# Optimization experiments

Measured on AMD Instinct MI355X. Metric: run time of the kernel, lower is better.

Reference implementation:

```python
import jax, jax.numpy as jnp
import numpy as np

DT_RANK = 64
N_STATES = 16


def selective_scan(u, delta, A, B, C, D):
    # u,delta: [b,l,d]; A: [d,n]; B,C: [b,l,n]; D: [d]
    dA = jnp.einsum('bld,dn->bldn', delta, A)
    dB_u = jnp.einsum('bld,bld,bln->bldn', delta, u, B)
    # shifted exclusive suffix-sum: cum[t] = sum_{s=t+1}^{L-1} dA[s]
    dA_shift = jnp.concatenate([dA[:, 1:], jnp.zeros_like(dA[:, :1])], axis=1)
    dA_cumsum = jnp.exp(jnp.flip(jnp.cumsum(jnp.flip(dA_shift, axis=1), axis=1), axis=1))
    xs = jnp.cumsum(dB_u * dA_cumsum, axis=1) / (dA_cumsum + 1e-12)
    y = jnp.einsum('bldn,bln->bld', xs, C)
    return y + u * D


def setup_inputs() -> dict:
    key = jax.random.key(0)
    ks = jax.random.split(key, 6)
    b, l, d = 2, 1024, 1024
    dt_rank, n = DT_RANK, N_STATES
    x = jax.random.normal(ks[0], (b, l, d), dtype=jnp.float32)
    # Dense kernels with glorot-ish scale
    W_x = jax.random.normal(ks[1], (d, dt_rank + 2 * n), dtype=jnp.float32) * (1.0 / np.sqrt(d))
    W_dt = jax.random.normal(ks[2], (dt_rank, d), dtype=jnp.float32) * (1.0 / np.sqrt(dt_rank))
    b_dt = jnp.zeros((d,), dtype=jnp.float32)
    # A_log = log(repeat(1..n, d)) as in S6.__init__
    A_log = jnp.log(jnp.tile(jnp.arange(1, n + 1, dtype=jnp.float32)[None, :], (d, 1)))
    D = jnp.ones((d,), dtype=jnp.float32)
    W_out = jax.random.normal(ks[3], (d, d), dtype=jnp.float32) * (1.0 / np.sqrt(d))
    b_out = jnp.zeros((d,), dtype=jnp.float32)
    return {"x": x, "W_x": W_x, "W_dt": W_dt, "b_dt": b_dt,
            "A_log": A_log, "D": D, "W_out": W_out, "b_out": b_out}


def reference(x, W_x, W_dt, b_dt, A_log, D, W_out, b_out):
    n = A_log.shape[1]
    A = -jnp.exp(A_log)                     # [d,n]
    x_dbl = jnp.einsum('bld,de->ble', x, W_x)  # [b,l,dt_rank+2n]
    delta = x_dbl[..., :DT_RANK]
    B = x_dbl[..., DT_RANK:DT_RANK + n]
    C = x_dbl[..., DT_RANK + n:]
    delta = jax.nn.softplus(jnp.einsum('blr,rd->bld', delta, W_dt) + b_dt)
    y = selective_scan(x, delta, A, B, C, D)
    return jnp.einsum('bld,de->ble', y, W_out) + b_out
```

## Files before the change

kernel.cpp:

```cpp
#include <hip/hip_runtime.h>
#include <hip/hip_bf16.h>

#define LSEQ 1024
#define DMODEL 1024
#define NSTATE 16
#define DTRANK 64
#define ECOL 96
#define MTOT 2048

typedef short s16x8 __attribute__((ext_vector_type(8)));
typedef float f32x4 __attribute__((ext_vector_type(4)));

#if __has_builtin(__builtin_amdgcn_exp2f)
#define EXP2F(x) __builtin_amdgcn_exp2f(x)
#else
#define EXP2F(x) exp2f(x)
#endif
#define LOG2E 1.4426950408889634

__device__ inline unsigned short f2bf(float f) {
    unsigned int u = __builtin_bit_cast(unsigned int, f);
    u += 0x7FFFu + ((u >> 16) & 1u);
    return (unsigned short)(u >> 16);
}
__device__ inline float bf2f(unsigned short h) {
    unsigned int u = ((unsigned int)h) << 16;
    return __builtin_bit_cast(float, u);
}

__device__ inline f32x4 shflup4(f32x4 v, int off) {
    f32x4 r;
    r[0] = __shfl_up(v[0], off, 64);
    r[1] = __shfl_up(v[1], off, 64);
    r[2] = __shfl_up(v[2], off, 64);
    r[3] = __shfl_up(v[3], off, 64);
    return r;
}

__global__ __launch_bounds__(256) void k_prep(const float* __restrict__ x,
                                              const float* __restrict__ Wx,
                                              const float* __restrict__ Wdt,
                                              const float* __restrict__ Wout,
                                              unsigned short* __restrict__ xTbf,
                                              unsigned short* __restrict__ WxTh,
                                              unsigned short* __restrict__ WxTl,
                                              unsigned short* __restrict__ WdtTh,
                                              unsigned short* __restrict__ WdtTl,
                                              unsigned short* __restrict__ WbfT) {
    __shared__ float t[64][65];
    int id = blockIdx.x;
    int tid = threadIdx.x;
    if (id < 512) {
        int d0 = (id & 15) * 64, m0 = (id >> 4) * 64;
        int tx = tid & 63, ty = tid >> 6;
#pragma unroll
        for (int j = 0; j < 64; j += 4)
            t[ty + j][tx] = x[(size_t)(m0 + ty + j) * 1024 + d0 + tx];
        __syncthreads();
#pragma unroll
        for (int j = 0; j < 64; j += 4)
            xTbf[(size_t)(d0 + ty + j) * 2048 + m0 + tx] = f2bf(t[tx][ty + j]);
    } else if (id < 512 + 96) {
        int id2 = id - 512;
        int e0 = (id2 % 3) * 32, k0 = (id2 / 3) * 32;
        int tx = tid & 31, ty = tid >> 5;
#pragma unroll
        for (int j = 0; j < 32; j += 8)
            t[ty + j][tx] = Wx[(size_t)(k0 + ty + j) * 96 + e0 + tx];
        __syncthreads();
#pragma unroll
        for (int j = 0; j < 32; j += 8) {
            float v = t[tx][ty + j];
            unsigned short h = f2bf(v);
            WxTh[(size_t)(e0 + ty + j) * 1024 + k0 + tx] = h;
            WxTl[(size_t)(e0 + ty + j) * 1024 + k0 + tx] = f2bf(v - bf2f(h));
        }
    } else if (id < 512 + 96 + 64) {
        int id3 = id - (512 + 96);
        int d0 = (id3 & 31) * 32, r0 = (id3 >> 5) * 32;
        int tx = tid & 31, ty = tid >> 5;
#pragma unroll
        for (int j = 0; j < 32; j += 8)
            t[ty + j][tx] = Wdt[(size_t)(r0 + ty + j) * 1024 + d0 + tx];
        __syncthreads();
#pragma unroll
        for (int j = 0; j < 32; j += 8) {
            float v = t[tx][ty + j];
            unsigned short h = f2bf(v);
            WdtTh[(size_t)(d0 + ty + j) * 64 + r0 + tx] = h;
            WdtTl[(size_t)(d0 + ty + j) * 64 + r0 + tx] = f2bf(v - bf2f(h));
        }
    } else {
        int id4 = id - (512 + 96 + 64);
        int e0 = (id4 & 15) * 64, k0 = (id4 >> 4) * 64;
        int tx = tid & 63, ty = tid >> 6;
#pragma unroll
        for (int j = 0; j < 64; j += 4)
            t[ty + j][tx] = Wout[(size_t)(k0 + ty + j) * 1024 + e0 + tx];
        __syncthreads();
#pragma unroll
        for (int j = 0; j < 64; j += 4)
            WbfT[(size_t)(e0 + ty + j) * 1024 + k0 + tx] = f2bf(t[tx][ty + j]);
    }
}

__global__ __launch_bounds__(256) void k_xdbl3(const float* __restrict__ x,
                                               const unsigned short* __restrict__ WxTh,
                                               const unsigned short* __restrict__ WxTl,
                                               float* __restrict__ part) {
    __shared__ unsigned short Ah[32 * 64], Al[32 * 64];
    __shared__ unsigned short Bh[96 * 64], Bl[96 * 64];
    int bm = (blockIdx.x >> 2) * 32;
    int slice = blockIdx.x & 3;
    int tid = threadIdx.x, lane = tid & 63, w = tid >> 6;
    int wm = w >> 1, wn = w & 1;
    int r = lane & 15, kb = lane >> 4;

    f32x4 acc[3];
#pragma unroll
    for (int nf = 0; nf < 3; ++nf) acc[nf] = (f32x4){0.f, 0.f, 0.f, 0.f};

#pragma unroll 1
    for (int kc = 0; kc < 4; ++kc) {
        int kbase = slice * 256 + kc * 64;
        __syncthreads();
        {
            int row = tid >> 3, cc = tid & 7;
            size_t src = (size_t)(bm + row) * 1024 + kbase + cc * 8;
            float4 v0 = *(const float4*)&x[src];
            float4 v1 = *(const float4*)&x[src + 4];
            float vv[8] = {v0.x, v0.y, v0.z, v0.w, v1.x, v1.y, v1.z, v1.w};
            s16x8 h, lo;
#pragma unroll
            for (int j = 0; j < 8; ++j) {
                unsigned short hb = f2bf(vv[j]);
                h[j] = (short)hb;
                lo[j] = (short)f2bf(vv[j] - bf2f(hb));
            }
            int dstB = row * 128 + ((cc * 16) ^ ((row & 7) << 4));
            *(s16x8*)((char*)Ah + dstB) = h;
            *(s16x8*)((char*)Al + dstB) = lo;
        }
#pragma unroll
        for (int j = 0; j < 3; ++j) {
            int c = tid + j * 256;
            int row = c >> 3, cc = c & 7;
            size_t src = (size_t)row * 1024 + kbase + cc * 8;
            int dstB = row * 128 + ((cc * 16) ^ ((row & 7) << 4));
            *(s16x8*)((char*)Bh + dstB) = *(const s16x8*)&WxTh[src];
            *(s16x8*)((char*)Bl + dstB) = *(const s16x8*)&WxTl[src];
        }
        __syncthreads();
#pragma unroll
        for (int ks = 0; ks < 2; ++ks) {
            int sw = (ks * 64 + kb * 16) ^ ((r & 7) << 4);
            s16x8 a_h = *(const s16x8*)((char*)Ah + (wm * 16 + r) * 128 + sw);
            s16x8 a_l = *(const s16x8*)((char*)Al + (wm * 16 + r) * 128 + sw);
#pragma unroll
            for (int nf = 0; nf < 3; ++nf) {
                int brow = wn * 48 + nf * 16 + r;
                s16x8 b_h = *(const s16x8*)((char*)Bh + brow * 128 + sw);
                s16x8 b_l = *(const s16x8*)((char*)Bl + brow * 128 + sw);
                acc[nf] = __builtin_amdgcn_mfma_f32_16x16x32_bf16(a_h, b_h, acc[nf], 0, 0, 0);
                acc[nf] = __builtin_amdgcn_mfma_f32_16x16x32_bf16(a_h, b_l, acc[nf], 0, 0, 0);
                acc[nf] = __builtin_amdgcn_mfma_f32_16x16x32_bf16(a_l, b_h, acc[nf], 0, 0, 0);
            }
        }
    }
    float* pb = part + (size_t)slice * 2048 * 96;
#pragma unroll
    for (int nf = 0; nf < 3; ++nf)
#pragma unroll
        for (int j = 0; j < 4; ++j)
            pb[(size_t)(bm + wm * 16 + kb * 4 + j) * 96 + wn * 48 + nf * 16 + r] = acc[nf][j];
}

__global__ __launch_bounds__(256) void k_delta2(const float* __restrict__ part,
                                                const unsigned short* __restrict__ WdtTh,
                                                const unsigned short* __restrict__ WdtTl,
                                                const float* __restrict__ bdt,
                                                float* __restrict__ deltaT,
                                                float* __restrict__ bpk,
                                                float* __restrict__ cpk) {
    __shared__ char pool[34816];
    unsigned short* Ah = (unsigned short*)pool;
    unsigned short* Al = (unsigned short*)(pool + 16384);
    float (*slab)[32][68] = (float (*)[32][68])pool;

    int bm = blockIdx.y * 128;
    int bn = blockIdx.x * 64;
    int tid = threadIdx.x, lane = tid & 63, w = tid >> 6;
    int wm = w >> 1, wn = w & 1;
    int r = lane & 15, kb = lane >> 4;

#pragma unroll
    for (int i = 0; i < 8; ++i) {
        int q = tid + i * 256;
        int row = q >> 4, c4 = q & 15;
        size_t off = (size_t)(bm + row) * 96 + c4 * 4;
        f32x4 v = *(const f32x4*)&part[off];
#pragma unroll
        for (int s = 1; s < 4; ++s) v += *(const f32x4*)&part[(size_t)s * 2048 * 96 + off];
        ushort4 h4, l4;
        h4.x = f2bf(v[0]); l4.x = f2bf(v[0] - bf2f(h4.x));
        h4.y = f2bf(v[1]); l4.y = f2bf(v[1] - bf2f(h4.y));
        h4.z = f2bf(v[2]); l4.z = f2bf(v[2] - bf2f(h4.z));
        h4.w = f2bf(v[3]); l4.w = f2bf(v[3] - bf2f(h4.w));
        int dstB = row * 128 + ((c4 * 8) ^ ((row & 7) << 4));
        *(ushort4*)((char*)Ah + dstB) = h4;
        *(ushort4*)((char*)Al + dstB) = l4;
    }
    if (blockIdx.x == 0) {
#pragma unroll
        for (int i = 0; i < 4; ++i) {
            int q = tid + i * 256;
            int row = q >> 3, c4 = q & 7;
            size_t off = (size_t)(bm + row) * 96 + 64 + c4 * 4;
            f32x4 v = *(const f32x4*)&part[off];
#pragma unroll
            for (int s = 1; s < 4; ++s) v += *(const f32x4*)&part[(size_t)s * 2048 * 96 + off];
            if (c4 < 4) *(f32x4*)&bpk[(size_t)(bm + row) * 16 + c4 * 4] = v;
            else        *(f32x4*)&cpk[(size_t)(bm + row) * 16 + (c4 - 4) * 4] = v;
        }
    }
    __syncthreads();

    f32x4 acc[4][2];
#pragma unroll
    for (int mf = 0; mf < 4; ++mf)
#pragma unroll
        for (int nf = 0; nf < 2; ++nf) acc[mf][nf] = (f32x4){0.f, 0.f, 0.f, 0.f};

#pragma unroll
    for (int ks = 0; ks < 2; ++ks) {
        int sw = (ks * 64 + kb * 16) ^ ((r & 7) << 4);
        s16x8 Afh[4], Afl[4], Bh[2], Bl[2];
#pragma unroll
        for (int mf = 0; mf < 4; ++mf) {
            int arow = wm * 64 + mf * 16 + r;
            Afh[mf] = *(const s16x8*)((char*)Ah + arow * 128 + sw);
            Afl[mf] = *(const s16x8*)((char*)Al + arow * 128 + sw);
        }
#pragma unroll
        for (int nf = 0; nf < 2; ++nf) {
            size_t b = (size_t)(bn + wn * 32 + nf * 16 + r) * 64 + ks * 32 + kb * 8;
            Bh[nf] = *(const s16x8*)&WdtTh[b];
            Bl[nf] = *(const s16x8*)&WdtTl[b];
        }
#pragma unroll
        for (int mf = 0; mf < 4; ++mf)
#pragma unroll
            for (int nf = 0; nf < 2; ++nf) {
                acc[mf][nf] = __builtin_amdgcn_mfma_f32_16x16x32_bf16(Afh[mf], Bh[nf], acc[mf][nf], 0, 0, 0);
                acc[mf][nf] = __builtin_amdgcn_mfma_f32_16x16x32_bf16(Afh[mf], Bl[nf], acc[mf][nf], 0, 0, 0);
                acc[mf][nf] = __builtin_amdgcn_mfma_f32_16x16x32_bf16(Afl[mf], Bh[nf], acc[mf][nf], 0, 0, 0);
            }
    }
    __syncthreads();

#pragma unroll
    for (int nf = 0; nf < 2; ++nf) {
        float bb = bdt[bn + wn * 32 + nf * 16 + r];
#pragma unroll
        for (int mf = 0; mf < 4; ++mf)
#pragma unroll
            for (int j = 0; j < 4; ++j) {
                float z = acc[mf][nf][j] + bb;
                float sp = fmaxf(z, 0.f) + log1pf(expf(-fabsf(z)));
                slab[w][nf * 16 + r][mf * 16 + kb * 4 + j] = sp;
            }
    }
#pragma unroll
    for (int i = 0; i < 8; ++i) {
        int idx = i * 64 + lane;
        int dl = idx >> 4, mq = (idx & 15) * 4;
        f32x4 v = *(const f32x4*)&slab[w][dl][mq];
        *(f32x4*)&deltaT[(size_t)(bn + wn * 32 + dl) * MTOT + bm + wm * 64 + mq] = v;
    }
}

__global__ __launch_bounds__(256) void k_scan3(const float* __restrict__ deltaT,
                                               const unsigned short* __restrict__ xTbf,
                                               const float* __restrict__ bpk,
                                               const float* __restrict__ cpk,
                                               const float* __restrict__ Alog,
                                               const float* __restrict__ Dp,
                                               unsigned short* __restrict__ yTbf) {
    __shared__ double csum[64];
    __shared__ double Rbef[64];
    __shared__ float TcL[64 * 20];
    __shared__ float syp[64 * 17];

    int tid = threadIdx.x;
    int c = tid >> 2, l = tid & 3;
    int w = tid >> 6, lane = tid & 63;
    int d = blockIdx.x & 1023, b = blockIdx.x >> 10;
    int m0 = b * 1024;

    const f32x4* dp = (const f32x4*)(deltaT + (size_t)d * MTOT + m0 + c * 16);
    const unsigned short* up = xTbf + (size_t)d * MTOT + m0 + c * 16;
    const f32x4* Bp = (const f32x4*)bpk + (size_t)(m0 + c * 16) * 4 + l;
    const f32x4* Cp = (const f32x4*)cpk + (size_t)(m0 + c * 16) * 4 + l;

    double dsum = 0.0;
#pragma unroll
    for (int i = 0; i < 4; ++i) {
        f32x4 v = dp[i];
        dsum += (double)v[0] + (double)v[1] + (double)v[2] + (double)v[3];
    }
    if (l == 0) csum[c] = dsum;
    __syncthreads();
    if (tid < 64) {
        double v = csum[tid];
#pragma unroll
        for (int off = 1; off < 64; off <<= 1) {
            double t = __shfl_down(v, off, 64);
            if (tid + off < 64) v += t;
        }
        Rbef[tid] = v;
    }
    __syncthreads();

    float Af2[4], Sb2[4];
    double Rb = Rbef[c];
#pragma unroll
    for (int j = 0; j < 4; ++j) {
        float Af = -__expf(Alog[d * NSTATE + 4 * l + j]);
        double A2 = (double)Af * LOG2E;
        Af2[j] = (float)A2;
        Sb2[j] = (float)(A2 * Rb);
    }
    float Dv = Dp[d];

    float P = 0.f;
    f32x4 Tn = {0.f, 0.f, 0.f, 0.f};
#pragma unroll 1
    for (int t4 = 0; t4 < 4; ++t4) {
        f32x4 rdv = dp[t4];
        ushort4 uv = *(const ushort4*)(up + t4 * 4);
        float ru[4] = {bf2f(uv.x), bf2f(uv.y), bf2f(uv.z), bf2f(uv.w)};
        f32x4 Bq[4];
#pragma unroll
        for (int k = 0; k < 4; ++k) Bq[k] = Bp[(t4 * 4 + k) * 4];
#pragma unroll
        for (int k = 0; k < 4; ++k) {
            float dlt = rdv[k];
            P += dlt;
            float du = dlt * ru[k];
#pragma unroll
            for (int j = 0; j < 4; ++j) {
                float e = EXP2F(fmaf(-Af2[j], P, Sb2[j]));
                Tn[j] = fmaf(du * Bq[k][j], e, Tn[j]);
            }
        }
    }
    *(f32x4*)&TcL[c * 20 + 4 * l] = Tn;
    __syncthreads();

    {
        f32x4 v = *(const f32x4*)&TcL[lane * 20 + 4 * w];
#pragma unroll
        for (int off = 1; off < 64; off <<= 1) {
            f32x4 t = shflup4(v, off);
            if (lane >= off) v += t;
        }
        f32x4 ex = shflup4(v, 1);
        if (lane == 0) ex = (f32x4){0.f, 0.f, 0.f, 0.f};
        *(f32x4*)&TcL[lane * 20 + 4 * w] = ex;
    }
    __syncthreads();
    f32x4 num = *(const f32x4*)&TcL[c * 20 + 4 * l];

    P = 0.f;
#pragma unroll 1
    for (int t4 = 0; t4 < 4; ++t4) {
        f32x4 rdv = dp[t4];
        ushort4 uv = *(const ushort4*)(up + t4 * 4);
        float ru[4] = {bf2f(uv.x), bf2f(uv.y), bf2f(uv.z), bf2f(uv.w)};
        f32x4 Bq[4], Cq[4];
#pragma unroll
        for (int k = 0; k < 4; ++k) {
            Bq[k] = Bp[(t4 * 4 + k) * 4];
            Cq[k] = Cp[(t4 * 4 + k) * 4];
        }
#pragma unroll
        for (int k = 0; k < 4; ++k) {
            float dlt = rdv[k];
            P += dlt;
            float du = dlt * ru[k];
            float psum = 0.f;
#pragma unroll
            for (int j = 0; j < 4; ++j) {
                float e = EXP2F(fmaf(-Af2[j], P, Sb2[j]));
                num[j] = fmaf(du * Bq[k][j], e, num[j]);
                float rr = __builtin_amdgcn_rcpf(e + 1e-12f);
                psum = fmaf(num[j] * rr, Cq[k][j], psum);
            }
            psum += __shfl_xor(psum, 1);
            psum += __shfl_xor(psum, 2);
            if (l == 0) syp[c * 17 + t4 * 4 + k] = fmaf(ru[k], Dv, psum);
        }
    }
    __syncthreads();
    {
        int cc = tid >> 2, oo = (tid & 3) * 4;
        const float* sp = &syp[cc * 17 + oo];
        ushort4 o;
        o.x = f2bf(sp[0]);
        o.y = f2bf(sp[1]);
        o.z = f2bf(sp[2]);
        o.w = f2bf(sp[3]);
        *reinterpret_cast<ushort4*>(&yTbf[(size_t)d * MTOT + m0 + tid * 4]) = o;
    }
}

__global__ __launch_bounds__(256) void k_ytr(const unsigned short* __restrict__ in,
                                             unsigned short* __restrict__ out) {
    __shared__ unsigned short t[64][66];
    int d0 = blockIdx.y * 64, m0 = blockIdx.x * 64;
    int tx = threadIdx.x & 63, ty = threadIdx.x >> 6;
#pragma unroll
    for (int j = 0; j < 64; j += 4)
        t[ty + j][tx] = in[(size_t)(d0 + ty + j) * MTOT + m0 + tx];
    __syncthreads();
#pragma unroll
    for (int j = 0; j < 64; j += 4)
        out[(size_t)(m0 + ty + j) * 1024 + d0 + tx] = t[tx][ty + j];
}

__global__ __launch_bounds__(256) void k_gemm(const unsigned short* __restrict__ A,
                                              const unsigned short* __restrict__ B,
                                              const float* __restrict__ bias,
                                              float* __restrict__ out) {
    __shared__ unsigned short As[64 * 64];
    __shared__ unsigned short Bs[64 * 64];
    const int GN = 1024, GK = 1024;
    int bm = blockIdx.y * 64;
    int bn = blockIdx.x * 64;
    int tid = threadIdx.x;
    int lane = tid & 63;
    int w = tid >> 6;
    int wm = w >> 1, wn = w & 1;
    int r = lane & 15, kb = lane >> 4;

    f32x4 acc[2][2];
#pragma unroll
    for (int mf = 0; mf < 2; ++mf)
#pragma unroll
        for (int nf = 0; nf < 2; ++nf) acc[mf][nf] = (f32x4){0.f, 0.f, 0.f, 0.f};

    s16x8 ra[2], rb[2];
    auto stage_load = [&](int k0) {
#pragma unroll
        for (int i = 0; i < 2; ++i) {
            int q = tid + i * 256;
            ra[i] = *reinterpret_cast<const s16x8*>(&A[(size_t)(bm + (q >> 3)) * GK + k0 + (q & 7) * 8]);
            rb[i] = *reinterpret_cast<const s16x8*>(&B[(size_t)(bn + (q >> 3)) * GK + k0 + (q & 7) * 8]);
        }
    };

    stage_load(0);
    for (int k0 = 0; k0 < GK; k0 += 64) {
        __syncthreads();
#pragma unroll
        for (int i = 0; i < 2; ++i) {
            int q = tid + i * 256;
            int row = q >> 3;
            int dstB = row * 128 + (((q & 7) * 16) ^ ((row & 7) << 4));
            *(s16x8*)((char*)As + dstB) = ra[i];
            *(s16x8*)((char*)Bs + dstB) = rb[i];
        }
        __syncthreads();
        if (k0 + 64 < GK) stage_load(k0 + 64);
#pragma unroll
        for (int ks = 0; ks < 2; ++ks) {
            int sw = (ks * 64 + kb * 16) ^ ((r & 7) << 4);
            s16x8 af[2], bfr[2];
#pragma unroll
            for (int mf = 0; mf < 2; ++mf)
                af[mf] = *(const s16x8*)((char*)As + (wm * 32 + mf * 16 + r) * 128 + sw);
#pragma unroll
            for (int nf = 0; nf < 2; ++nf)
                bfr[nf] = *(const s16x8*)((char*)Bs + (wn * 32 + nf * 16 + r) * 128 + sw);
#pragma unroll
            for (int mf = 0; mf < 2; ++mf)
#pragma unroll
                for (int nf = 0; nf < 2; ++nf)
                    acc[mf][nf] = __builtin_amdgcn_mfma_f32_16x16x32_bf16(af[mf], bfr[nf], acc[mf][nf], 0, 0, 0);
        }
    }
#pragma unroll
    for (int nf = 0; nf < 2; ++nf) {
        float bb = bias[bn + wn * 32 + nf * 16 + r];
#pragma unroll
        for (int mf = 0; mf < 2; ++mf)
#pragma unroll
            for (int j = 0; j < 4; ++j)
                out[(size_t)(bm + wm * 32 + mf * 16 + kb * 4 + j) * GN + bn + wn * 32 + nf * 16 + r] =
                    acc[mf][nf][j] + bb;
    }
}

extern "C" void kernel_launch(void* const* d_in, const int* in_sizes, int n_in,
                              void* d_out, int out_size, void* d_ws, size_t ws_size,
                              hipStream_t stream) {
    const float* x    = (const float*)d_in[0];
    const float* Wx   = (const float*)d_in[1];
    const float* Wdt  = (const float*)d_in[2];
    const float* bdt  = (const float*)d_in[3];
    const float* Alog = (const float*)d_in[4];
    const float* Dp   = (const float*)d_in[5];
    const float* Wout = (const float*)d_in[6];
    const float* bout = (const float*)d_in[7];
    float* out = (float*)d_out;

    float* deltaT = (float*)d_ws;
    float* bpk    = deltaT + 1024 * 2048;
    float* cpk    = bpk + 2048 * 16;
    float* part   = cpk + 2048 * 16;
    unsigned short* xTbf  = (unsigned short*)(part + 4 * 2048 * 96);
    unsigned short* WxTh  = xTbf + 1024 * 2048;
    unsigned short* WxTl  = WxTh + 96 * 1024;
    unsigned short* WdtTh = WxTl + 96 * 1024;
    unsigned short* WdtTl = WdtTh + 1024 * 64;
    unsigned short* yTbf  = WdtTl + 1024 * 64;
    unsigned short* ybf   = yTbf + 1024 * 2048;
    unsigned short* WbfT  = ybf + 2048 * 1024;

    k_prep<<<928, 256, 0, stream>>>(x, Wx, Wdt, Wout, xTbf,
                                    WxTh, WxTl, WdtTh, WdtTl, WbfT);
    k_xdbl3<<<256, 256, 0, stream>>>(x, WxTh, WxTl, part);
    k_delta2<<<dim3(16, 16), 256, 0, stream>>>(part, WdtTh, WdtTl, bdt, deltaT, bpk, cpk);
    k_scan3<<<2048, 256, 0, stream>>>(deltaT, xTbf, bpk, cpk, Alog, Dp, yTbf);
    k_ytr<<<dim3(32, 16), 256, 0, stream>>>(yTbf, ybf);
    k_gemm<<<dim3(16, 32), 256, 0, stream>>>(ybf, WbfT, bout, out);
}
```

Measured before the change: 75.74 us.

## Fuse y transpose into output GEMM by loading transposed tiles directly

Removes the separate k_ytr transpose kernel and its intermediate buffer, and has the output GEMM read the d-major yT buffer directly. Pairs of k rows are packed into 32-bit words in a padded shared-memory tile so the MFMA A-fragments can be assembled with four scalar LDS reads. This drops one kernel launch and a full 4MB read+write round trip. In exchange, the A loads become narrower 8-byte reads and fragment assembly uses more LDS instructions.

Measured after the change: 74.03 us. -2.3%, faster.

```diff
diff --git a/kernel.cpp b/kernel.cpp
--- a/kernel.cpp
+++ b/kernel.cpp
@@ -10,6 +10,7 @@
 
 typedef short s16x8 __attribute__((ext_vector_type(8)));
 typedef float f32x4 __attribute__((ext_vector_type(4)));
+typedef unsigned int u32x4 __attribute__((ext_vector_type(4)));
 
 #if __has_builtin(__builtin_amdgcn_exp2f)
 #define EXP2F(x) __builtin_amdgcn_exp2f(x)
@@ -414,25 +415,11 @@
     }
 }
 
-__global__ __launch_bounds__(256) void k_ytr(const unsigned short* __restrict__ in,
-                                             unsigned short* __restrict__ out) {
-    __shared__ unsigned short t[64][66];
-    int d0 = blockIdx.y * 64, m0 = blockIdx.x * 64;
-    int tx = threadIdx.x & 63, ty = threadIdx.x >> 6;
-#pragma unroll
-    for (int j = 0; j < 64; j += 4)
-        t[ty + j][tx] = in[(size_t)(d0 + ty + j) * MTOT + m0 + tx];
-    __syncthreads();
-#pragma unroll
-    for (int j = 0; j < 64; j += 4)
-        out[(size_t)(m0 + ty + j) * 1024 + d0 + tx] = t[tx][ty + j];
-}
-
-__global__ __launch_bounds__(256) void k_gemm(const unsigned short* __restrict__ A,
+__global__ __launch_bounds__(256) void k_gemm(const unsigned short* __restrict__ yT,
                                               const unsigned short* __restrict__ B,
                                               const float* __restrict__ bias,
                                               float* __restrict__ out) {
-    __shared__ unsigned short As[64 * 64];
+    __shared__ unsigned int P[32 * 68];
     __shared__ unsigned short Bs[64 * 64];
     const int GN = 1024, GK = 1024;
     int bm = blockIdx.y * 64;
@@ -449,13 +436,16 @@
 #pragma unroll
         for (int nf = 0; nf < 2; ++nf) acc[mf][nf] = (f32x4){0.f, 0.f, 0.f, 0.f};
 
-    s16x8 ra[2], rb[2];
+    ushort4 rya[2], ryb[2];
+    s16x8 rbv[2];
     auto stage_load = [&](int k0) {
 #pragma unroll
         for (int i = 0; i < 2; ++i) {
-            int q = tid + i * 256;
-            ra[i] = *reinterpret_cast<const s16x8*>(&A[(size_t)(bm + (q >> 3)) * GK + k0 + (q & 7) * 8]);
-            rb[i] = *reinterpret_cast<const s16x8*>(&B[(size_t)(bn + (q >> 3)) * GK + k0 + (q & 7) * 8]);
+            int slot = tid + i * 256;
+            int p = slot >> 4, mq = (slot & 15) * 4;
+            rya[i] = *(const ushort4*)&yT[(size_t)(k0 + 2 * p) * MTOT + bm + mq];
+            ryb[i] = *(const ushort4*)&yT[(size_t)(k0 + 2 * p + 1) * MTOT + bm + mq];
+            rbv[i] = *(const s16x8*)&B[(size_t)(bn + (slot >> 3)) * GK + k0 + (slot & 7) * 8];
         }
     };
 
@@ -464,11 +454,17 @@
         __syncthreads();
 #pragma unroll
         for (int i = 0; i < 2; ++i) {
-            int q = tid + i * 256;
-            int row = q >> 3;
-            int dstB = row * 128 + (((q & 7) * 16) ^ ((row & 7) << 4));
-            *(s16x8*)((char*)As + dstB) = ra[i];
-            *(s16x8*)((char*)Bs + dstB) = rb[i];
+            int slot = tid + i * 256;
+            int p = slot >> 4, mq = (slot & 15) * 4;
+            u32x4 pk;
+            pk[0] = (unsigned int)rya[i].x | ((unsigned int)ryb[i].x << 16);
+            pk[1] = (unsigned int)rya[i].y | ((unsigned int)ryb[i].y << 16);
+            pk[2] = (unsigned int)rya[i].z | ((unsigned int)ryb[i].z << 16);
+            pk[3] = (unsigned int)rya[i].w | ((unsigned int)ryb[i].w << 16);
+            *(u32x4*)&P[p * 68 + mq] = pk;
+            int row = slot >> 3;
+            int dstB = row * 128 + (((slot & 7) * 16) ^ ((row & 7) << 4));
+            *(s16x8*)((char*)Bs + dstB) = rbv[i];
         }
         __syncthreads();
         if (k0 + 64 < GK) stage_load(k0 + 64);
@@ -477,8 +473,15 @@
             int sw = (ks * 64 + kb * 16) ^ ((r & 7) << 4);
             s16x8 af[2], bfr[2];
 #pragma unroll
-            for (int mf = 0; mf < 2; ++mf)
-                af[mf] = *(const s16x8*)((char*)As + (wm * 32 + mf * 16 + r) * 128 + sw);
+            for (int mf = 0; mf < 2; ++mf) {
+                int base = (ks * 16 + kb * 4) * 68 + wm * 32 + mf * 16 + r;
+                u32x4 av;
+                av[0] = P[base];
+                av[1] = P[base + 68];
+                av[2] = P[base + 136];
+                av[3] = P[base + 204];
+                af[mf] = __builtin_bit_cast(s16x8, av);
+            }
 #pragma unroll
             for (int nf = 0; nf < 2; ++nf)
                 bfr[nf] = *(const s16x8*)((char*)Bs + (wn * 32 + nf * 16 + r) * 128 + sw);
@@ -524,14 +527,12 @@
     unsigned short* WdtTh = WxTl + 96 * 1024;
     unsigned short* WdtTl = WdtTh + 1024 * 64;
     unsigned short* yTbf  = WdtTl + 1024 * 64;
-    unsigned short* ybf   = yTbf + 1024 * 2048;
-    unsigned short* WbfT  = ybf + 2048 * 1024;
+    unsigned short* WbfT  = yTbf + 1024 * 2048;
 
     k_prep<<<928, 256, 0, stream>>>(x, Wx, Wdt, Wout, xTbf,
                                     WxTh, WxTl, WdtTh, WdtTl, WbfT);
     k_xdbl3<<<256, 256, 0, stream>>>(x, WxTh, WxTl, part);
     k_delta2<<<dim3(16, 16), 256, 0, stream>>>(part, WdtTh, WdtTl, bdt, deltaT, bpk, cpk);
     k_scan3<<<2048, 256, 0, stream>>>(deltaT, xTbf, bpk, cpk, Alog, Dp, yTbf);
-    k_ytr<<<dim3(32, 16), 256, 0, stream>>>(yTbf, ybf);
-    k_gemm<<<dim3(16, 32), 256, 0, stream>>>(ybf, WbfT, bout, out);
-}
+    k_gemm<<<dim3(16, 32), 256, 0, stream>>>(yTbf, WbfT, bout, out);
+}
```
